# Kernel tuning notes

Measured on AMD Instinct MI355X. Metric: run time of the kernel, lower is better.

The kernel has to match this reference:

```python
import jax, jax.numpy as jnp
import numpy as np

# dims: batch, channels, classes, transform channels, spatial
B, C, NCLS, T, H, W = 4, 512, 19, 256, 128, 128
NH, NW, PH, PW = 8, 8, 16, 16  # patch grid and patch size (H=NH*PH, no padding)


def conv1x1(x, w):
    # x: (b,c,h,w), w: (o,c) -> (b,o,h,w)
    return jnp.einsum('oc,bchw->bohw', w, x)


def conv3x3(x, w):
    return jax.lax.conv_general_dilated(x, w, (1, 1), 'SAME',
                                        dimension_numbers=('NCHW', 'OIHW', 'NCHW'))


def bn(x, s, b):
    # eval-mode BatchNorm folded into per-channel scale/shift
    return x * s[None, :, None, None] + b[None, :, None, None]


def relu6(x):
    return jnp.clip(x, 0.0, 6.0)


def patch_split(x):
    b, c = x.shape[0], x.shape[1]
    return x.reshape(b, c, NH, PH, NW, PW).transpose(0, 2, 4, 1, 3, 5).reshape(b * NH * NW, c, PH, PW)


def patch_recover(x):
    c = x.shape[1]
    return x.reshape(B, NH, NW, c, PH, PW).transpose(0, 3, 1, 4, 2, 5).reshape(B, c, H, W)


def setup_inputs() -> dict:
    key = jax.random.key(0)
    ks = jax.random.split(key, 40)

    def n(i, shape, s=1.0):
        return jax.random.normal(ks[i], shape, jnp.float32) * s

    def u(i, shape):
        return jax.random.uniform(ks[i], shape, jnp.float32, 0.5, 1.5)

    return {
        'feat': n(0, (B, C, H, W)),
        'global_center': n(1, (B, C, C), 1.0 / np.sqrt(C)),
        'w_proj': n(2, (C, C), 0.05), 'b_proj': n(3, (C,), 0.01),
        'w_dec': n(4, (NCLS, C), 0.05), 'b_dec': n(5, (NCLS,), 0.01),
        'q1_w': n(6, (T, C), 0.05), 'q1_s': u(7, (T,)), 'q1_b': n(8, (T,), 0.01),
        'q2_w': n(9, (T, T), 0.05), 'q2_s': u(10, (T,)), 'q2_b': n(11, (T,), 0.01),
        'k1_w': n(12, (T, C), 0.05), 'k1_s': u(13, (T,)), 'k1_b': n(14, (T,), 0.01),
        'k2_w': n(15, (T, T), 0.05), 'k2_s': u(16, (T,)), 'k2_b': n(17, (T,), 0.01),
        'v_w': n(18, (T, C), 0.05), 'v_s': u(19, (T,)), 'v_b': n(20, (T,), 0.01),
        'o_w': n(21, (C, T), 0.05), 'o_s': u(22, (C,)), 'o_b': n(23, (C,), 0.01),
        'cat1_w': n(24, (C, 2 * C, 3, 3), 0.02), 'cat1_s': u(25, (C,)), 'cat1_b': n(26, (C,), 0.01),
        'cat2_w': n(27, (C, C, 3, 3), 0.02), 'cat2_s': u(28, (C,)), 'cat2_b': n(29, (C,), 0.01),
    }


def reference(feat, global_center, w_proj, b_proj, w_dec, b_dec,
              q1_w, q1_s, q1_b, q2_w, q2_s, q2_b,
              k1_w, k1_s, k1_b, k2_w, k2_s, k2_b,
              v_w, v_s, v_b, o_w, o_s, o_b,
              cat1_w, cat1_s, cat1_b, cat2_w, cat2_s, cat2_b):
    relu = jax.nn.relu
    # class logits
    pred = conv1x1(feat, w_dec) + b_dec[None, :, None, None]          # (B,NCLS,H,W)
    residual = feat
    f = conv1x1(feat, w_proj) + b_proj[None, :, None, None]
    f = jnp.einsum('bcd,bdn->bcn', global_center, f.reshape(B, C, H * W)).reshape(B, C, H, W)
    f = relu6(residual + f)
    # patch split: N = B*NH*NW patches of (PH,PW)
    pf = patch_split(f)        # (N,C,PH,PW)
    pp = patch_split(pred)     # (N,NCLS,PH,PW)
    N = pf.shape[0]
    pp_flat = pp.reshape(N, NCLS, PH * PW)
    # LocalClassGatherModule (scale=1): per-class softmax over patch pixels
    probs = jax.nn.softmax(pp_flat, axis=2)                           # (N,NCLS,hw)
    ctx = jnp.einsum('nkp,ncp->nkc', probs, pf.reshape(N, C, PH * PW))  # (N,NCLS,C)
    # Recover: gather per-pixel class context via argmax label
    idx = jnp.argmax(pp_flat, axis=1)                                 # (N,hw)
    local = jnp.take_along_axis(ctx, idx[:, :, None], axis=1)         # (N,hw,C)
    local = local.transpose(0, 2, 1).reshape(N, C, PH, PW)
    # SelfAttentionBlock (correlate_net); BN in eval mode
    q = relu(bn(conv1x1(pf, q1_w), q1_s, q1_b))
    q = relu(bn(conv1x1(q, q2_w), q2_s, q2_b))
    k = relu(bn(conv1x1(local, k1_w), k1_s, k1_b))
    k = relu(bn(conv1x1(k, k2_w), k2_s, k2_b))
    v = relu(bn(conv1x1(local, v_w), v_s, v_b))
    qf = q.reshape(N, T, PH * PW).transpose(0, 2, 1)   # (N,hw,T)
    kf = k.reshape(N, T, PH * PW)                      # (N,T,hw)
    vf = v.reshape(N, T, PH * PW).transpose(0, 2, 1)   # (N,hw,T)
    sim = jax.nn.softmax(jnp.einsum('npt,ntq->npq', qf, kf) * T ** -0.5, axis=-1)
    cxt = jnp.einsum('npq,nqt->npt', sim, vf).transpose(0, 2, 1).reshape(N, T, PH, PW)
    cxt = relu(bn(conv1x1(cxt, o_w), o_s, o_b))        # (N,C,PH,PW)
    new_feat = patch_recover(cxt)                      # (B,C,H,W)
    # cat_conv (Dropout2d is identity in eval)
    out = jnp.concatenate([residual, new_feat], axis=1)
    out = relu6(bn(conv3x3(out, cat1_w), cat1_s, cat1_b))
    out = relu6(bn(conv3x3(out, cat2_w), cat2_s, cat2_b))
    return out
```

## Files before the change

### kernel.cpp

```cpp
#include <hip/hip_runtime.h>
#include <hip/hip_bf16.h>

typedef __attribute__((ext_vector_type(8))) short bf16x8;
typedef __attribute__((ext_vector_type(4))) float f32x4;

#define DEVFN __device__ __forceinline__

DEVFN float b2f(short s) {
    union { unsigned u; float f; } x;
    x.u = ((unsigned)(unsigned short)s) << 16;
    return x.f;
}
DEVFN unsigned short f2b(float f) {
    unsigned u = __float_as_uint(f);
    unsigned r = (u + 0x7FFFu + ((u >> 16) & 1u)) >> 16;
    return (unsigned short)r;
}
DEVFN void gload16(const __hip_bfloat16* g, __hip_bfloat16* l) {
    __builtin_amdgcn_global_load_lds(
        (const __attribute__((address_space(1))) void*)g,
        (__attribute__((address_space(3))) void*)l, 16, 0, 0);
}

struct InPtrs { const void* p[27]; };

#define ARENA_TOT 1981976

__global__ void detect_k(const void* q1s, int* flag)
{
    const int ln = threadIdx.x;
    const unsigned short* s = (const unsigned short*)q1s;
    float v = b2f((short)s[ln]);
    int ok = (v >= 0.35f && v <= 1.7f) ? 1 : 0;
    for (int off = 32; off >= 1; off >>= 1) ok += __shfl_xor(ok, off, 64);
    if (ln == 0) *flag = (ok >= 56) ? 1 : 0;
}

__global__ __launch_bounds__(256) void cvt_arena(
    InPtrs ip, const int* __restrict__ flagp, unsigned short* __restrict__ arena)
{
    constexpr int SSZ[27] = {1048576,262144,512,9728,19,131072,256,256,65536,
        256,256,131072,256,256,65536,256,256,131072,256,256,131072,512,512,
        512,512,512,512};
    constexpr int SB[27] = {0,1048576,1310720,1311232,1320960,1320984,1452056,
        1452312,1452568,1518104,1518360,1518616,1649688,1649944,1650200,
        1715736,1715992,1716248,1847320,1847576,1847832,1978904,1979416,
        1979928,1980440,1980952,1981464};
    const int flag = *flagp;
    const int gid = blockIdx.x * 256 + threadIdx.x;
    const int stride = gridDim.x * 256;
    for (int s = 0; s < 27; ++s) {
        unsigned short* op = arena + SB[s];
        if (flag) {
            const unsigned short* in = (const unsigned short*)ip.p[s];
            for (int i = gid; i < SSZ[s]; i += stride) op[i] = in[i];
        } else {
            const float* in = (const float*)ip.p[s];
            for (int i = gid; i < SSZ[s]; i += stride) op[i] = f2b(in[i]);
        }
    }
}

__global__ __launch_bounds__(256) void feat_transpose(
    const void* __restrict__ in, const int* __restrict__ flagp,
    unsigned short* __restrict__ out)
{
    const int flag = *flagp;
    __shared__ unsigned short tile[64 * 65];
    const int tid = threadIdx.x;
    const int c0 = blockIdx.x * 64, r0 = blockIdx.y * 64;
    const size_t ibase = (size_t)blockIdx.z * 8388608;
    #pragma unroll
    for (int i = 0; i < 16; ++i) {
        int L = i * 256 + tid;
        int r = L >> 6, c = L & 63;
        size_t idx = ibase + (size_t)(r0 + r) * 16384 + c0 + c;
        tile[r * 65 + c] = flag ? ((const unsigned short*)in)[idx]
                                : f2b(((const float*)in)[idx]);
    }
    __syncthreads();
    #pragma unroll
    for (int i = 0; i < 16; ++i) {
        int L = i * 256 + tid;
        int cc = L >> 6, rr = L & 63;
        out[ibase + (size_t)(c0 + cc) * 512 + r0 + rr] = tile[rr * 65 + cc];
    }
}

__global__ __launch_bounds__(256) void transpose_k(
    const __hip_bfloat16* __restrict__ in, __hip_bfloat16* __restrict__ out,
    int R, int Cc)
{
    __shared__ __hip_bfloat16 tile[64 * 65];
    const int tid = threadIdx.x;
    const int c0 = blockIdx.x * 64, r0 = blockIdx.y * 64;
    #pragma unroll
    for (int i = 0; i < 16; ++i) {
        int L = i * 256 + tid;
        int r = L >> 6, c = L & 63;
        tile[r * 65 + c] = in[(size_t)(r0 + r) * Cc + c0 + c];
    }
    __syncthreads();
    #pragma unroll
    for (int i = 0; i < 16; ++i) {
        int L = i * 256 + tid;
        int cc = L >> 6, rr = L & 63;
        out[(size_t)(c0 + cc) * R + r0 + rr] = tile[rr * 65 + cc];
    }
}

__global__ void reorder_w(const void* __restrict__ w, const int* __restrict__ flagp,
                          unsigned short* __restrict__ wr, int CinN)
{
    const int flag = *flagp;
    int i = blockIdx.x * 256 + threadIdx.x;
    int total = 512 * CinN * 9;
    if (i >= total) return;
    int tap = i / (512 * CinN);
    int rem = i - tap * 512 * CinN;
    int o = rem / CinN;
    int c = rem - o * CinN;
    size_t si = ((size_t)o * CinN + c) * 9 + tap;
    wr[i] = flag ? ((const unsigned short*)w)[si] : f2b(((const float*)w)[si]);
}

__global__ void vb_k(const __hip_bfloat16* __restrict__ gc,
                     const __hip_bfloat16* __restrict__ bp,
                     float* __restrict__ vb)
{
    int i = blockIdx.x * 256 + threadIdx.x;
    const short* row = (const short*)gc + (size_t)i * 512;
    const short* bps = (const short*)bp;
    float a = 0.f;
    for (int d = 0; d < 512; ++d) a += b2f(row[d]) * b2f(bps[d]);
    vb[i] = a;
}

template <int EPI>
__global__ __launch_bounds__(256) void gemm_nt(
    const __hip_bfloat16* __restrict__ A, const __hip_bfloat16* __restrict__ Bw,
    __hip_bfloat16* __restrict__ Co, int K, int N,
    const __hip_bfloat16* __restrict__ sv, const __hip_bfloat16* __restrict__ bv,
    const float* __restrict__ vbp, const __hip_bfloat16* __restrict__ resid,
    long sA, long sB, long sC, int sV)
{
    __shared__ __hip_bfloat16 As[4096];
    __shared__ __hip_bfloat16 Bs[4096];
    const int tid = threadIdx.x;
    const int nb = blockIdx.x, mb = blockIdx.y, bz = blockIdx.z;
    A += (size_t)bz * sA;
    Bw += (size_t)bz * sB;
    Co += (size_t)bz * sC;
    if (EPI == 2) { resid += (size_t)bz * sC; vbp += (size_t)bz * (size_t)sV; }
    const int lane = tid & 63, wave = tid >> 6;
    const int wm = (wave >> 1) << 6, wn = (wave & 1) << 6;
    const int m15 = lane & 15, quad = lane >> 4;
    const int srow = lane >> 2;
    const int sgoff = ((lane & 3) ^ ((lane >> 2) & 3) ^ ((lane >> 4) & 3)) * 8;
    const int fsw = (quad ^ (m15 & 3) ^ ((m15 >> 2) & 3)) * 8;
    f32x4 acc[4][4];
    #pragma unroll
    for (int i = 0; i < 4; ++i)
        #pragma unroll
        for (int j = 0; j < 4; ++j) {
            acc[i][j][0] = 0.f; acc[i][j][1] = 0.f;
            acc[i][j][2] = 0.f; acc[i][j][3] = 0.f;
        }
    const size_t abase = (size_t)mb * 128 * K;
    const size_t bbase = (size_t)nb * 128 * K;
    for (int k0 = 0; k0 < K; k0 += 32) {
        __syncthreads();
        #pragma unroll
        for (int j = 0; j < 2; ++j) {
            const int i = wave * 2 + j;
            const int row = i * 16 + srow;
            gload16(A + abase + (size_t)row * K + k0 + sgoff, &As[i * 512]);
            gload16(Bw + bbase + (size_t)row * K + k0 + sgoff, &Bs[i * 512]);
        }
        __syncthreads();
        bf16x8 af[4], bfv[4];
        #pragma unroll
        for (int mt = 0; mt < 4; ++mt)
            af[mt] = *(const bf16x8*)&As[(wm + mt * 16 + m15) * 32 + fsw];
        #pragma unroll
        for (int nt = 0; nt < 4; ++nt)
            bfv[nt] = *(const bf16x8*)&Bs[(wn + nt * 16 + m15) * 32 + fsw];
        #pragma unroll
        for (int mt = 0; mt < 4; ++mt)
            #pragma unroll
            for (int nt = 0; nt < 4; ++nt)
                acc[mt][nt] = __builtin_amdgcn_mfma_f32_16x16x32_bf16(
                    af[mt], bfv[nt], acc[mt][nt], 0, 0, 0);
    }
    unsigned short* outp = (unsigned short*)Co;
    #pragma unroll
    for (int nt = 0; nt < 4; ++nt) {
        const int n = nb * 128 + wn + nt * 16 + m15;
        float sc = 0.f, sh = 0.f, vbn = 0.f;
        if (EPI == 1) { sc = b2f(((const short*)sv)[n]); sh = b2f(((const short*)bv)[n]); }
        if (EPI == 2) vbn = vbp[n];
        #pragma unroll
        for (int mt = 0; mt < 4; ++mt) {
            const int mb2 = mb * 128 + wm + mt * 16 + quad * 4;
            #pragma unroll
            for (int r = 0; r < 4; ++r) {
                const int m = mb2 + r;
                float v = acc[mt][nt][r];
                if (EPI == 1) {
                    v = fmaxf(v * sc + sh, 0.f);
                } else if (EPI == 2) {
                    v += vbn + b2f(((const short*)resid)[(size_t)m * N + n]);
                    v = fminf(fmaxf(v, 0.f), 6.f);
                }
                outp[(size_t)m * N + n] = f2b(v);
            }
        }
    }
}

template <int CIN, bool CHMAJOR>
__global__ __launch_bounds__(256) void conv3x3k(
    const __hip_bfloat16* __restrict__ in0, const __hip_bfloat16* __restrict__ in1,
    const __hip_bfloat16* __restrict__ Wt, void* __restrict__ outp,
    const __hip_bfloat16* __restrict__ sv, const __hip_bfloat16* __restrict__ bv,
    const int* __restrict__ flagp)
{
    __shared__ __hip_bfloat16 smem[8448];
    __hip_bfloat16* As = smem;
    __hip_bfloat16* Bs = smem + 4096;
    const int tid = threadIdx.x;
    const int L = blockIdx.x;
    const int xcd = L & 7;
    const int g = L >> 3;
    const int nb = g & 3;
    const int h = xcd * 16 + ((g >> 2) & 15);
    const int b = g >> 6;
    const int lane = tid & 63, wave = tid >> 6;
    const int wm = (wave >> 1) << 6, wn = (wave & 1) << 6;
    const int m15 = lane & 15, quad = lane >> 4;
    const int r0 = tid >> 2, akoff = (tid & 3) << 3;
    const int asw = (((tid & 3) ^ ((tid >> 2) & 3) ^ ((tid >> 4) & 3))) * 8;
    const int srow = lane >> 2;
    const int sgoff = ((lane & 3) ^ ((lane >> 2) & 3) ^ ((lane >> 4) & 3)) * 8;
    const int fsw = (quad ^ (m15 & 3) ^ ((m15 >> 2) & 3)) * 8;
    f32x4 acc[4][4];
    #pragma unroll
    for (int i = 0; i < 4; ++i)
        #pragma unroll
        for (int j = 0; j < 4; ++j) {
            acc[i][j][0] = 0.f; acc[i][j][1] = 0.f;
            acc[i][j][2] = 0.f; acc[i][j][3] = 0.f;
        }
    const size_t pixbase = (size_t)b * 16384 + (size_t)h * 128;
    for (int tap = 0; tap < 9; ++tap) {
        const int dy = tap / 3 - 1, dx = tap % 3 - 1;
        const int hh = h + dy;
        const bool hok = (unsigned)hh < 128u;
        const __hip_bfloat16* wtap = Wt + (size_t)tap * 512 * CIN;
        const size_t rowbase = (size_t)b * 16384 + (size_t)hh * 128;
        for (int c0 = 0; c0 < CIN; c0 += 32) {
            const __hip_bfloat16* src = (CIN > 512 && c0 >= 512) ? in1 : in0;
            const int cl = c0 & 511;
            bf16x8 a0, a1;
            {
                int ww = r0 + dx;
                if (hok && (unsigned)ww < 128u)
                    a0 = *(const bf16x8*)&src[(rowbase + ww) * 512 + cl + akoff];
                else
                    for (int j = 0; j < 8; ++j) a0[j] = 0;
                ww = r0 + 64 + dx;
                if (hok && (unsigned)ww < 128u)
                    a1 = *(const bf16x8*)&src[(rowbase + ww) * 512 + cl + akoff];
                else
                    for (int j = 0; j < 8; ++j) a1[j] = 0;
            }
            __syncthreads();
            #pragma unroll
            for (int j = 0; j < 2; ++j) {
                const int i = wave * 2 + j;
                const int row = i * 16 + srow;
                gload16(wtap + (size_t)(nb * 128 + row) * CIN + c0 + sgoff,
                        &Bs[i * 512]);
            }
            *(bf16x8*)&As[r0 * 32 + asw] = a0;
            *(bf16x8*)&As[(r0 + 64) * 32 + asw] = a1;
            __syncthreads();
            bf16x8 af[4], bfv[4];
            #pragma unroll
            for (int mt = 0; mt < 4; ++mt)
                af[mt] = *(const bf16x8*)&As[(wm + mt * 16 + m15) * 32 + fsw];
            #pragma unroll
            for (int nt = 0; nt < 4; ++nt)
                bfv[nt] = *(const bf16x8*)&Bs[(wn + nt * 16 + m15) * 32 + fsw];
            #pragma unroll
            for (int mt = 0; mt < 4; ++mt)
                #pragma unroll
                for (int nt = 0; nt < 4; ++nt)
                    acc[mt][nt] = __builtin_amdgcn_mfma_f32_16x16x32_bf16(
                        af[mt], bfv[nt], acc[mt][nt], 0, 0, 0);
        }
    }
    if (!CHMAJOR) {
        unsigned short* op = (unsigned short*)outp;
        #pragma unroll
        for (int nt = 0; nt < 4; ++nt) {
            const int n = nb * 128 + wn + nt * 16 + m15;
            const float sc = b2f(((const short*)sv)[n]);
            const float sh = b2f(((const short*)bv)[n]);
            #pragma unroll
            for (int mt = 0; mt < 4; ++mt) {
                #pragma unroll
                for (int r = 0; r < 4; ++r) {
                    const int wc = wm + mt * 16 + quad * 4 + r;
                    float v = fminf(fmaxf(acc[mt][nt][r] * sc + sh, 0.f), 6.f);
                    op[(pixbase + wc) * 512 + n] = f2b(v);
                }
            }
        }
    } else {
        const int flag = *flagp;
        unsigned short* sm16 = (unsigned short*)smem;
        __syncthreads();
        #pragma unroll
        for (int half = 0; half < 2; ++half) {
            if ((wn >> 6) == half) {
                #pragma unroll
                for (int nt = 0; nt < 4; ++nt) {
                    const int nl = nt * 16 + m15;
                    const int n = nb * 128 + half * 64 + nl;
                    const float sc = b2f(((const short*)sv)[n]);
                    const float sh = b2f(((const short*)bv)[n]);
                    #pragma unroll
                    for (int mt = 0; mt < 4; ++mt) {
                        #pragma unroll
                        for (int r = 0; r < 4; ++r) {
                            const int wc = wm + mt * 16 + quad * 4 + r;
                            float v = fminf(fmaxf(acc[mt][nt][r] * sc + sh, 0.f), 6.f);
                            sm16[nl * 130 + wc] = f2b(v);
                        }
                    }
                }
            }
            __syncthreads();
            const int nr = tid >> 2, qt = tid & 3;
            const int och = nb * 128 + half * 64 + nr;
            const size_t gb = ((size_t)(b * 512 + och)) * 16384 +
                              (size_t)h * 128 + qt * 32;
            const unsigned short* srw = sm16 + nr * 130 + qt * 32;
            if (flag) {
                unsigned short* oh = (unsigned short*)outp;
                #pragma unroll
                for (int j = 0; j < 4; ++j)
                    *(bf16x8*)&oh[gb + j * 8] = *(const bf16x8*)&srw[j * 8];
            } else {
                float* of = (float*)outp;
                #pragma unroll
                for (int j = 0; j < 32; j += 4) {
                    f32x4 v;
                    v[0] = b2f((short)srw[j]);
                    v[1] = b2f((short)srw[j + 1]);
                    v[2] = b2f((short)srw[j + 2]);
                    v[3] = b2f((short)srw[j + 3]);
                    *(f32x4*)&of[gb + j] = v;
                }
            }
            __syncthreads();
        }
    }
}

__global__ __launch_bounds__(256) void patch_pred(
    const __hip_bfloat16* __restrict__ featT, const __hip_bfloat16* __restrict__ f2T,
    const __hip_bfloat16* __restrict__ w_dec, const __hip_bfloat16* __restrict__ b_dec,
    float* __restrict__ ctx_g, int* __restrict__ cnt_g)
{
    __shared__ __hip_bfloat16 wds[19 * 512];
    __shared__ float pp[19 * 256];
    __shared__ int cnt[19];
    const int tid = threadIdx.x;
    const int n = blockIdx.x;
    const int b = n >> 6, nh = (n >> 3) & 7, nw = n & 7;
    const int ph = tid >> 4, pw = tid & 15;
    const size_t pbase = (size_t)b * 16384 + (size_t)nh * 2048 + (size_t)nw * 16;
    const size_t g = pbase + (size_t)ph * 128 + pw;
    if (tid < 19) cnt[tid] = 0;
    for (int i = tid; i < 19 * 512; i += 256) wds[i] = w_dec[i];
    __syncthreads();
    float lg[19];
    #pragma unroll
    for (int k = 0; k < 19; ++k) lg[k] = b2f(((const short*)b_dec)[k]);
    const __hip_bfloat16* xrow = featT + g * 512;
    for (int c0 = 0; c0 < 512; c0 += 8) {
        bf16x8 x8 = *(const bf16x8*)&xrow[c0];
        float xf[8];
        #pragma unroll
        for (int j = 0; j < 8; ++j) xf[j] = b2f(x8[j]);
        #pragma unroll
        for (int k = 0; k < 19; ++k) {
            bf16x8 w8 = *(const bf16x8*)&wds[k * 512 + c0];
            #pragma unroll
            for (int j = 0; j < 8; ++j) lg[k] += xf[j] * b2f(w8[j]);
        }
    }
    int best = 0;
    float bvv = lg[0];
    #pragma unroll
    for (int k = 1; k < 19; ++k)
        if (lg[k] > bvv) { bvv = lg[k]; best = k; }
    atomicAdd(&cnt[best], 1);
    #pragma unroll
    for (int k = 0; k < 19; ++k) pp[k * 256 + tid] = lg[k];
    __syncthreads();
    if (tid < 19) cnt_g[n * 19 + tid] = cnt[tid];
    const int wv = tid >> 6, ln = tid & 63;
    for (int k = wv; k < 19; k += 4) {
        float v0 = pp[k * 256 + ln], v1 = pp[k * 256 + 64 + ln];
        float v2 = pp[k * 256 + 128 + ln], v3 = pp[k * 256 + 192 + ln];
        float mx = fmaxf(fmaxf(v0, v1), fmaxf(v2, v3));
        for (int off = 32; off >= 1; off >>= 1) mx = fmaxf(mx, __shfl_xor(mx, off, 64));
        float e0 = __expf(v0 - mx), e1 = __expf(v1 - mx);
        float e2 = __expf(v2 - mx), e3 = __expf(v3 - mx);
        float s = e0 + e1 + e2 + e3;
        for (int off = 32; off >= 1; off >>= 1) s += __shfl_xor(s, off, 64);
        float inv = 1.f / s;
        pp[k * 256 + ln] = e0 * inv;
        pp[k * 256 + 64 + ln] = e1 * inv;
        pp[k * 256 + 128 + ln] = e2 * inv;
        pp[k * 256 + 192 + ln] = e3 * inv;
    }
    __syncthreads();
    const short* f2s = (const short*)f2T;
    for (int o = tid; o < 19 * 512; o += 256) {
        const int k = o >> 9, c = o & 511;
        const short* p0 = f2s + pbase * 512 + c;
        const float* ppk = &pp[k * 256];
        float a = 0.f;
        for (int pr = 0; pr < 16; ++pr) {
            const short* prow = p0 + (size_t)pr * 65536;
            const float* ppr = ppk + pr * 16;
            #pragma unroll
            for (int pc = 0; pc < 16; ++pc)
                a += ppr[pc] * b2f(prow[(size_t)pc * 512]);
        }
        ctx_g[(size_t)n * 9728 + o] = a;
    }
}

__global__ __launch_bounds__(256) void patch_kv(
    const float* __restrict__ ctx_g,
    const __hip_bfloat16* __restrict__ k1w, const __hip_bfloat16* __restrict__ k1s,
    const __hip_bfloat16* __restrict__ k1b,
    const __hip_bfloat16* __restrict__ k2w, const __hip_bfloat16* __restrict__ k2s,
    const __hip_bfloat16* __restrict__ k2b,
    const __hip_bfloat16* __restrict__ vw, const __hip_bfloat16* __restrict__ vs,
    const __hip_bfloat16* __restrict__ vbq,
    const __hip_bfloat16* __restrict__ ow,
    float* __restrict__ k2c_g, float* __restrict__ OV_g)
{
    __shared__ float ctx_s[19 * 512];
    __shared__ float tmp_s[256 * 20];
    const int tid = threadIdx.x;
    const int n = blockIdx.x;
    for (int i = tid; i < 19 * 512; i += 256) ctx_s[i] = ctx_g[(size_t)n * 9728 + i];
    __syncthreads();
    const int t = tid;
    float a[19];
    #pragma unroll
    for (int k = 0; k < 19; ++k) a[k] = 0.f;
    for (int c0 = 0; c0 < 512; c0 += 8) {
        bf16x8 w8 = *(const bf16x8*)&k1w[t * 512 + c0];
        float wf[8];
        #pragma unroll
        for (int j = 0; j < 8; ++j) wf[j] = b2f(w8[j]);
        #pragma unroll
        for (int k = 0; k < 19; ++k) {
            f32x4 ca = *(const f32x4*)&ctx_s[k * 512 + c0];
            f32x4 cb = *(const f32x4*)&ctx_s[k * 512 + c0 + 4];
            a[k] += wf[0]*ca[0] + wf[1]*ca[1] + wf[2]*ca[2] + wf[3]*ca[3]
                  + wf[4]*cb[0] + wf[5]*cb[1] + wf[6]*cb[2] + wf[7]*cb[3];
        }
    }
    {
        float sc = b2f(((const short*)k1s)[t]), sh = b2f(((const short*)k1b)[t]);
        #pragma unroll
        for (int k = 0; k < 19; ++k) tmp_s[t * 20 + k] = fmaxf(a[k] * sc + sh, 0.f);
    }
    __syncthreads();
    #pragma unroll
    for (int k = 0; k < 19; ++k) a[k] = 0.f;
    for (int t0 = 0; t0 < 256; t0 += 8) {
        bf16x8 w8 = *(const bf16x8*)&k2w[t * 256 + t0];
        #pragma unroll
        for (int j = 0; j < 8; ++j) {
            float wf = b2f(w8[j]);
            #pragma unroll
            for (int k = 0; k < 19; ++k) a[k] += wf * tmp_s[(t0 + j) * 20 + k];
        }
    }
    {
        float sc = b2f(((const short*)k2s)[t]), sh = b2f(((const short*)k2b)[t]);
        #pragma unroll
        for (int k = 0; k < 19; ++k)
            k2c_g[((size_t)n * 256 + t) * 19 + k] = fmaxf(a[k] * sc + sh, 0.f);
    }
    __syncthreads();
    #pragma unroll
    for (int k = 0; k < 19; ++k) a[k] = 0.f;
    for (int c0 = 0; c0 < 512; c0 += 8) {
        bf16x8 w8 = *(const bf16x8*)&vw[t * 512 + c0];
        float wf[8];
        #pragma unroll
        for (int j = 0; j < 8; ++j) wf[j] = b2f(w8[j]);
        #pragma unroll
        for (int k = 0; k < 19; ++k) {
            f32x4 ca = *(const f32x4*)&ctx_s[k * 512 + c0];
            f32x4 cb = *(const f32x4*)&ctx_s[k * 512 + c0 + 4];
            a[k] += wf[0]*ca[0] + wf[1]*ca[1] + wf[2]*ca[2] + wf[3]*ca[3]
                  + wf[4]*cb[0] + wf[5]*cb[1] + wf[6]*cb[2] + wf[7]*cb[3];
        }
    }
    {
        float sc = b2f(((const short*)vs)[t]), sh = b2f(((const short*)vbq)[t]);
        #pragma unroll
        for (int k = 0; k < 19; ++k) tmp_s[t * 20 + k] = fmaxf(a[k] * sc + sh, 0.f);
    }
    __syncthreads();
    for (int cc = t; cc < 512; cc += 256) {
        float o[19];
        #pragma unroll
        for (int k = 0; k < 19; ++k) o[k] = 0.f;
        for (int t0 = 0; t0 < 256; t0 += 8) {
            bf16x8 w8 = *(const bf16x8*)&ow[cc * 256 + t0];
            #pragma unroll
            for (int j = 0; j < 8; ++j) {
                float wf = b2f(w8[j]);
                #pragma unroll
                for (int k = 0; k < 19; ++k) o[k] += wf * tmp_s[(t0 + j) * 20 + k];
            }
        }
        #pragma unroll
        for (int k = 0; k < 19; ++k) OV_g[((size_t)n * 512 + cc) * 19 + k] = o[k];
    }
}

__global__ __launch_bounds__(256) void patch_attn(
    const __hip_bfloat16* __restrict__ qT, const float* __restrict__ k2c_g,
    const float* __restrict__ OV_g, const int* __restrict__ cnt_g,
    const __hip_bfloat16* __restrict__ os, const __hip_bfloat16* __restrict__ ob,
    __hip_bfloat16* __restrict__ nfT)
{
    __shared__ float k2s[256 * 19];
    __shared__ float OVs[512 * 19];
    __shared__ float osf[512], obf[512];
    __shared__ int cnts[19];
    const int tid = threadIdx.x;
    const int n = blockIdx.x;
    const int b = n >> 6, nh = (n >> 3) & 7, nw = n & 7;
    const int ph = tid >> 4, pw = tid & 15;
    const size_t g = (size_t)b * 16384 + (size_t)(nh * 16 + ph) * 128 + (nw * 16 + pw);
    for (int i = tid; i < 4864; i += 256) k2s[i] = k2c_g[(size_t)n * 4864 + i];
    for (int i = tid; i < 9728; i += 256) OVs[i] = OV_g[(size_t)n * 9728 + i];
    for (int i = tid; i < 512; i += 256) {
        osf[i] = b2f(((const short*)os)[i]);
        obf[i] = b2f(((const short*)ob)[i]);
    }
    if (tid < 19) cnts[tid] = cnt_g[n * 19 + tid];
    __syncthreads();
    float L[19];
    #pragma unroll
    for (int k = 0; k < 19; ++k) L[k] = 0.f;
    const short* qrow = (const short*)qT + g * 256;
    for (int t0 = 0; t0 < 256; t0 += 8) {
        bf16x8 q8 = *(const bf16x8*)&qrow[t0];
        #pragma unroll
        for (int j = 0; j < 8; ++j) {
            float qj = b2f(q8[j]);
            #pragma unroll
            for (int k = 0; k < 19; ++k) L[k] += qj * k2s[(t0 + j) * 19 + k];
        }
    }
    #pragma unroll
    for (int k = 0; k < 19; ++k) L[k] *= 0.0625f;
    float m = -1e30f;
    #pragma unroll
    for (int k = 0; k < 19; ++k)
        if (cnts[k] > 0) m = fmaxf(m, L[k]);
    float wgt[19], Z = 0.f;
    #pragma unroll
    for (int k = 0; k < 19; ++k) {
        float e = (cnts[k] > 0) ? (float)cnts[k] * __expf(L[k] - m) : 0.f;
        wgt[k] = e;
        Z += e;
    }
    float iz = 1.f / Z;
    #pragma unroll
    for (int k = 0; k < 19; ++k) wgt[k] *= iz;
    unsigned short* orow = (unsigned short*)nfT + g * 512;
    for (int c = 0; c < 512; c += 2) {
        float v0 = 0.f, v1 = 0.f;
        #pragma unroll
        for (int k = 0; k < 19; ++k) {
            v0 += wgt[k] * OVs[c * 19 + k];
            v1 += wgt[k] * OVs[(c + 1) * 19 + k];
        }
        v0 = fmaxf(osf[c] * v0 + obf[c], 0.f);
        v1 = fmaxf(osf[c + 1] * v1 + obf[c + 1], 0.f);
        unsigned pack = (unsigned)f2b(v0) | ((unsigned)f2b(v1) << 16);
        *(unsigned*)&orow[c] = pack;
    }
}

extern "C" void kernel_launch(void* const* d_in, const int* in_sizes, int n_in,
                              void* d_out, int out_size, void* d_ws, size_t ws_size,
                              hipStream_t stream)
{
    (void)in_sizes; (void)n_in; (void)out_size; (void)ws_size;

    char* ws = (char*)d_ws;
    constexpr size_t MiB = 1024ul * 1024;
    constexpr size_t O_W0   = 0;
    constexpr size_t O_W1   = 64 * MiB;
    constexpr size_t O_W2   = 96 * MiB;
    constexpr size_t O_w1r  = 128 * MiB;
    constexpr size_t O_w2r  = O_w1r + 9ul * 512 * 1024 * 2;
    constexpr size_t O_wpT  = O_w2r + 9ul * 512 * 512 * 2;
    constexpr size_t O_Mm   = O_wpT + 512ul * 512 * 2;
    constexpr size_t O_vb   = O_Mm + 4ul * 512 * 512 * 2;
    constexpr size_t O_ctx  = O_vb + 8192;
    constexpr size_t O_cnt  = O_ctx + 256ul * 19 * 512 * 4;
    constexpr size_t O_ar   = O_cnt + 32768;
    constexpr size_t O_flag = O_ar + (size_t)ARENA_TOT * 2;

    unsigned short* arena = (unsigned short*)(ws + O_ar);
    int*            flag  = (int*)(ws + O_flag);
    __hip_bfloat16* featT = (__hip_bfloat16*)d_out;
    __hip_bfloat16* f2T   = (__hip_bfloat16*)(ws + O_W0);
    __hip_bfloat16* nfT   = (__hip_bfloat16*)(ws + O_W0);
    __hip_bfloat16* q1T   = (__hip_bfloat16*)(ws + O_W1);
    float*          k2c   = (float*)(ws + O_W1);
    float*          OV    = (float*)(ws + O_W1 + 256ul * 256 * 19 * 4);
    __hip_bfloat16* c1T   = (__hip_bfloat16*)(ws + O_W1);
    __hip_bfloat16* qT    = (__hip_bfloat16*)(ws + O_W2);
    unsigned short* w1r   = (unsigned short*)(ws + O_w1r);
    unsigned short* w2r   = (unsigned short*)(ws + O_w2r);
    __hip_bfloat16* wpT   = (__hip_bfloat16*)(ws + O_wpT);
    __hip_bfloat16* Mmat  = (__hip_bfloat16*)(ws + O_Mm);
    float*          vb    = (float*)(ws + O_vb);
    float*          ctx   = (float*)(ws + O_ctx);
    int*            cnt   = (int*)(ws + O_cnt);

    const int AB_gc = 0, AB_wproj = 1048576, AB_bproj = 1310720,
        AB_wdec = 1311232, AB_bdec = 1320960, AB_q1w = 1320984,
        AB_q1s = 1452056, AB_q1b = 1452312, AB_q2w = 1452568,
        AB_q2s = 1518104, AB_q2b = 1518360, AB_k1w = 1518616,
        AB_k1s = 1649688, AB_k1b = 1649944, AB_k2w = 1650200,
        AB_k2s = 1715736, AB_k2b = 1715992, AB_vw = 1716248,
        AB_vs = 1847320, AB_vb = 1847576, AB_ow = 1847832,
        AB_os = 1978904, AB_ob = 1979416, AB_c1s = 1979928,
        AB_c1b = 1980440, AB_c2s = 1980952, AB_c2b = 1981464;
    #define AR(off) ((__hip_bfloat16*)(arena + (off)))

    InPtrs ip;
    {
        const int idx[27] = {1,2,3,4,5,6,7,8,9,10,11,12,13,14,15,16,17,18,19,
                             20,21,22,23,25,26,28,29};
        for (int i = 0; i < 27; ++i) ip.p[i] = d_in[idx[i]];
    }

    detect_k<<<dim3(1), 64, 0, stream>>>(d_in[7], flag);
    cvt_arena<<<dim3(1024), 256, 0, stream>>>(ip, flag, arena);
    feat_transpose<<<dim3(256, 8, 4), 256, 0, stream>>>(d_in[0], flag,
                                                        (unsigned short*)featT);
    transpose_k<<<dim3(8, 8, 1), 256, 0, stream>>>(AR(AB_wproj), wpT, 512, 512);
    reorder_w<<<dim3((512 * 1024 * 9 + 255) / 256), 256, 0, stream>>>(
        d_in[24], flag, w1r, 1024);
    reorder_w<<<dim3((512 * 512 * 9 + 255) / 256), 256, 0, stream>>>(
        d_in[27], flag, w2r, 512);
    vb_k<<<dim3(8), 256, 0, stream>>>(AR(AB_gc), AR(AB_bproj), vb);
    gemm_nt<0><<<dim3(4, 4, 4), 256, 0, stream>>>(
        AR(AB_gc), wpT, Mmat, 512, 512, nullptr, nullptr, nullptr, nullptr,
        512L * 512, 0L, 512L * 512, 0);
    gemm_nt<2><<<dim3(4, 128, 4), 256, 0, stream>>>(
        featT, Mmat, f2T, 512, 512, nullptr, nullptr, vb, featT,
        16384L * 512, 512L * 512, 16384L * 512, 512);
    patch_pred<<<dim3(256), 256, 0, stream>>>(featT, f2T, AR(AB_wdec),
                                              AR(AB_bdec), ctx, cnt);
    gemm_nt<1><<<dim3(2, 512, 1), 256, 0, stream>>>(
        f2T, AR(AB_q1w), q1T, 512, 256, AR(AB_q1s), AR(AB_q1b),
        nullptr, nullptr, 0L, 0L, 0L, 0);
    gemm_nt<1><<<dim3(2, 512, 1), 256, 0, stream>>>(
        q1T, AR(AB_q2w), qT, 256, 256, AR(AB_q2s), AR(AB_q2b),
        nullptr, nullptr, 0L, 0L, 0L, 0);
    patch_kv<<<dim3(256), 256, 0, stream>>>(
        ctx, AR(AB_k1w), AR(AB_k1s), AR(AB_k1b), AR(AB_k2w), AR(AB_k2s),
        AR(AB_k2b), AR(AB_vw), AR(AB_vs), AR(AB_vb), AR(AB_ow), k2c, OV);
    patch_attn<<<dim3(256), 256, 0, stream>>>(qT, k2c, OV, cnt, AR(AB_os),
                                              AR(AB_ob), nfT);
    conv3x3k<1024, false><<<dim3(2048), 256, 0, stream>>>(
        featT, nfT, (const __hip_bfloat16*)w1r, c1T, AR(AB_c1s), AR(AB_c1b), flag);
    conv3x3k<512, true><<<dim3(2048), 256, 0, stream>>>(
        c1T, c1T, (const __hip_bfloat16*)w2r, d_out, AR(AB_c2s), AR(AB_c2b), flag);
}
```

Baseline: 2.115 ms.

## Reuse one staged input row across three horizontal taps in conv3x3

```diff
diff --git a/kernel.cpp b/kernel.cpp
--- a/kernel.cpp
+++ b/kernel.cpp
@@ -155,9 +155,7 @@
     const int lane = tid & 63, wave = tid >> 6;
     const int wm = (wave >> 1) << 6, wn = (wave & 1) << 6;
     const int m15 = lane & 15, quad = lane >> 4;
-    const int srow = lane >> 2;
-    const int sgoff = ((lane & 3) ^ ((lane >> 2) & 3) ^ ((lane >> 4) & 3)) * 8;
-    const int fsw = (quad ^ (m15 & 3) ^ ((m15 >> 2) & 3)) * 8;
+    const int srow = lane >> 2, sseg = (lane & 3) << 3;
     f32x4 acc[4][4];
     #pragma unroll
     for (int i = 0; i < 4; ++i)
@@ -174,17 +172,17 @@
         for (int j = 0; j < 2; ++j) {
             const int i = wave * 2 + j;
             const int row = i * 16 + srow;
-            gload16(A + abase + (size_t)row * K + k0 + sgoff, &As[i * 512]);
-            gload16(Bw + bbase + (size_t)row * K + k0 + sgoff, &Bs[i * 512]);
+            gload16(A + abase + (size_t)row * K + k0 + sseg, &As[i * 512]);
+            gload16(Bw + bbase + (size_t)row * K + k0 + sseg, &Bs[i * 512]);
         }
         __syncthreads();
         bf16x8 af[4], bfv[4];
         #pragma unroll
         for (int mt = 0; mt < 4; ++mt)
-            af[mt] = *(const bf16x8*)&As[(wm + mt * 16 + m15) * 32 + fsw];
+            af[mt] = *(const bf16x8*)&As[(wm + mt * 16 + m15) * 32 + quad * 8];
         #pragma unroll
         for (int nt = 0; nt < 4; ++nt)
-            bfv[nt] = *(const bf16x8*)&Bs[(wn + nt * 16 + m15) * 32 + fsw];
+            bfv[nt] = *(const bf16x8*)&Bs[(wn + nt * 16 + m15) * 32 + quad * 8];
         #pragma unroll
         for (int mt = 0; mt < 4; ++mt)
             #pragma unroll
@@ -225,9 +223,9 @@
     const __hip_bfloat16* __restrict__ sv, const __hip_bfloat16* __restrict__ bv,
     const int* __restrict__ flagp)
 {
-    __shared__ __hip_bfloat16 smem[8448];
+    __shared__ __hip_bfloat16 smem[16448];
     __hip_bfloat16* As = smem;
-    __hip_bfloat16* Bs = smem + 4096;
+    __hip_bfloat16* Bs = smem + 4160;
     const int tid = threadIdx.x;
     const int L = blockIdx.x;
     const int xcd = L & 7;
@@ -238,11 +236,7 @@
     const int lane = tid & 63, wave = tid >> 6;
     const int wm = (wave >> 1) << 6, wn = (wave & 1) << 6;
     const int m15 = lane & 15, quad = lane >> 4;
-    const int r0 = tid >> 2, akoff = (tid & 3) << 3;
-    const int asw = (((tid & 3) ^ ((tid >> 2) & 3) ^ ((tid >> 4) & 3))) * 8;
-    const int srow = lane >> 2;
-    const int sgoff = ((lane & 3) ^ ((lane >> 2) & 3) ^ ((lane >> 4) & 3)) * 8;
-    const int fsw = (quad ^ (m15 & 3) ^ ((m15 >> 2) & 3)) * 8;
+    const int r0 = tid >> 2, sg8 = (tid & 3) << 3;
     f32x4 acc[4][4];
     #pragma unroll
     for (int i = 0; i < 4; ++i)
@@ -252,52 +246,69 @@
             acc[i][j][2] = 0.f; acc[i][j][3] = 0.f;
         }
     const size_t pixbase = (size_t)b * 16384 + (size_t)h * 128;
-    for (int tap = 0; tap < 9; ++tap) {
-        const int dy = tap / 3 - 1, dx = tap % 3 - 1;
+    for (int dy = -1; dy <= 1; ++dy) {
         const int hh = h + dy;
-        const bool hok = (unsigned)hh < 128u;
-        const __hip_bfloat16* wtap = Wt + (size_t)tap * 512 * CIN;
+        if ((unsigned)hh >= 128u) continue;
         const size_t rowbase = (size_t)b * 16384 + (size_t)hh * 128;
+        const __hip_bfloat16* wdy = Wt + (size_t)(dy + 1) * 3 * 512 * CIN;
         for (int c0 = 0; c0 < CIN; c0 += 32) {
             const __hip_bfloat16* src = (CIN > 512 && c0 >= 512) ? in1 : in0;
-            const int cl = c0 & 511;
-            bf16x8 a0, a1;
+            const int cl = (c0 & 511) + sg8;
+            bf16x8 a0, a1, a2;
             {
-                int ww = r0 + dx;
-                if (hok && (unsigned)ww < 128u)
-                    a0 = *(const bf16x8*)&src[(rowbase + ww) * 512 + cl + akoff];
+                int px = r0 - 1;
+                if ((unsigned)px < 128u)
+                    a0 = *(const bf16x8*)&src[(rowbase + px) * 512 + cl];
                 else
                     for (int j = 0; j < 8; ++j) a0[j] = 0;
-                ww = r0 + 64 + dx;
-                if (hok && (unsigned)ww < 128u)
-                    a1 = *(const bf16x8*)&src[(rowbase + ww) * 512 + cl + akoff];
+                px = r0 + 63;
+                if ((unsigned)px < 128u)
+                    a1 = *(const bf16x8*)&src[(rowbase + px) * 512 + cl];
                 else
                     for (int j = 0; j < 8; ++j) a1[j] = 0;
+                if (tid < 8) {
+                    px = (tid >> 2) + 127;
+                    if ((unsigned)px < 128u)
+                        a2 = *(const bf16x8*)&src[(rowbase + px) * 512 + cl];
+                    else
+                        for (int j = 0; j < 8; ++j) a2[j] = 0;
+                }
             }
             __syncthreads();
             #pragma unroll
-            for (int j = 0; j < 2; ++j) {
-                const int i = wave * 2 + j;
-                const int row = i * 16 + srow;
-                gload16(wtap + (size_t)(nb * 128 + row) * CIN + c0 + sgoff,
-                        &Bs[i * 512]);
+            for (int m = 0; m < 6; ++m) {
+                const int cidx = wave * 6 + m;
+                const int t = cidx >> 3;
+                const int j = cidx & 7;
+                const int row = nb * 128 + j * 16 + (lane >> 2);
+                gload16(wdy + (size_t)t * 512 * CIN + (size_t)row * CIN + c0
+                            + ((lane & 3) << 3),
+                        &Bs[t * 4096 + j * 512]);
             }
-            *(bf16x8*)&As[r0 * 32 + asw] = a0;
-            *(bf16x8*)&As[(r0 + 64) * 32 + asw] = a1;
+            *(bf16x8*)&As[r0 * 32 + sg8] = a0;
+            *(bf16x8*)&As[(r0 + 64) * 32 + sg8] = a1;
+            if (tid < 8)
+                *(bf16x8*)&As[((tid >> 2) + 128) * 32 + sg8] = a2;
             __syncthreads();
-            bf16x8 af[4], bfv[4];
-            #pragma unroll
-            for (int mt = 0; mt < 4; ++mt)
-                af[mt] = *(const bf16x8*)&As[(wm + mt * 16 + m15) * 32 + fsw];
-            #pragma unroll
-            for (int nt = 0; nt < 4; ++nt)
-                bfv[nt] = *(const bf16x8*)&Bs[(wn + nt * 16 + m15) * 32 + fsw];
-            #pragma unroll
-            for (int mt = 0; mt < 4; ++mt)
+            #pragma unroll
+            for (int t = 0; t < 3; ++t) {
+                bf16x8 af[4], bfv[4];
+                #pragma unroll
+                for (int mt = 0; mt < 4; ++mt)
+                    af[mt] = *(const bf16x8*)&As[(wm + mt * 16 + m15 + t) * 32
+                                                 + quad * 8];
                 #pragma unroll
                 for (int nt = 0; nt < 4; ++nt)
-                    acc[mt][nt] = __builtin_amdgcn_mfma_f32_16x16x32_bf16(
-                        af[mt], bfv[nt], acc[mt][nt], 0, 0, 0);
+                    bfv[nt] = *(const bf16x8*)&Bs[t * 4096
+                                                  + (wn + nt * 16 + m15) * 32
+                                                  + quad * 8];
+                #pragma unroll
+                for (int mt = 0; mt < 4; ++mt)
+                    #pragma unroll
+                    for (int nt = 0; nt < 4; ++nt)
+                        acc[mt][nt] = __builtin_amdgcn_mfma_f32_16x16x32_bf16(
+                            af[mt], bfv[nt], acc[mt][nt], 0, 0, 0);
+            }
         }
     }
     if (!CHMAJOR) {
```

New measurement: 1.858 ms. -12.2%, faster.
